# Optimization experiments

Measured on AMD Instinct MI355X. Metric: run time of the kernel, lower is better.

Reference implementation:

```python
import jax, jax.numpy as jnp
import numpy as np

B, S, D, H = 2, 2048, 128, 8  # batch, seq, num_hidden(=head dim), num_heads
EPS = 1e-5


def setup_inputs() -> dict:
    key = jax.random.key(0)
    ks = jax.random.split(key, 12)
    sc = 0.02
    return {
        "query": jax.random.normal(ks[0], (B, S, D), dtype=jnp.float32),
        "Wq": jax.random.normal(ks[1], (2 * H * D, D), dtype=jnp.float32) * sc,
        "bq": jnp.zeros((2 * H * D,), dtype=jnp.float32),
        "Wk": jax.random.normal(ks[2], (2 * H * D, D), dtype=jnp.float32) * sc,
        "bk": jnp.zeros((2 * H * D,), dtype=jnp.float32),
        "Wv": jax.random.normal(ks[3], (H * D, D), dtype=jnp.float32) * sc,
        "bv": jnp.zeros((H * D,), dtype=jnp.float32),
        "Wo": jax.random.normal(ks[4], (D, H * D), dtype=jnp.float32) * sc,
        "bo": jnp.zeros((D,), dtype=jnp.float32),
        "gn_w": jnp.ones((H,), dtype=jnp.float32),
        "gn_b": jnp.zeros((H,), dtype=jnp.float32),
        "lam": jax.random.uniform(ks[5], (), dtype=jnp.float32),
    }


def reference(query, Wq, bq, Wk, bk, Wv, bv, Wo, bo, gn_w, gn_b, lam):
    # Faithful to the torch module: the .view calls are raw reshapes (no
    # transpose), d_k=1 so scale is 1, mask=None path (no causal mask),
    # dropout in eval mode, _lambda == _lambda_init == lam.
    q = (query @ Wq.T + bq).reshape(B, H, S, 2 * D)
    k = (query @ Wk.T + bk).reshape(B, H, S, 2 * D)
    v = (query @ Wv.T + bv).reshape(B, H, S, D)
    q1, q2 = q[..., :D], q[..., D:]
    k1, k2 = k[..., :D], k[..., D:]
    s1 = jnp.einsum("bhqd,bhkd->bhqk", q1, k1)  # / sqrt(d_k=1)
    s2 = jnp.einsum("bhqd,bhkd->bhqk", q2, k2)
    attn = jax.nn.softmax(s1, axis=-1) - lam * jax.nn.softmax(s2, axis=-1)
    out = jnp.einsum("bhqk,bhkd->bhqd", attn, v)          # (B,H,S,D)
    out = out.transpose(0, 2, 1, 3).reshape(B, H, S, D)   # faithful raw reshape
    # GroupNorm(num_groups=H, num_channels=H): normalize per (b, h) over (S, D)
    mean = out.mean(axis=(2, 3), keepdims=True)
    var = out.var(axis=(2, 3), keepdims=True)
    out = (out - mean) * jax.lax.rsqrt(var + EPS)
    out = out * gn_w[None, :, None, None] + gn_b[None, :, None, None]
    out = out * (1.0 - lam)
    # torch.cat([out[:, i] for i in range(H)], dim=-1) -> (B, S, H*D)
    out = out.transpose(0, 2, 1, 3).reshape(B, S, H * D)
    return out @ Wo.T + bo
```

## Files before the change

### kernel.cpp

```cpp
#include <hip/hip_runtime.h>

typedef __bf16 bf16x8 __attribute__((ext_vector_type(8)));
typedef __bf16 bf16x4 __attribute__((ext_vector_type(4)));
typedef float  f32x4  __attribute__((ext_vector_type(4)));

#define MFMA16(a,b,c) __builtin_amdgcn_mfma_f32_16x16x32_bf16((a),(b),(c),0,0,0)

__device__ __forceinline__ bf16x8 cvt8(float4 a, float4 b) {
  bf16x8 v;
  v[0]=(__bf16)a.x; v[1]=(__bf16)a.y; v[2]=(__bf16)a.z; v[3]=(__bf16)a.w;
  v[4]=(__bf16)b.x; v[5]=(__bf16)b.y; v[6]=(__bf16)b.z; v[7]=(__bf16)b.w;
  return v;
}
__device__ __forceinline__ bf16x4 cvt4(float4 a) {
  bf16x4 v;
  v[0]=(__bf16)a.x; v[1]=(__bf16)a.y; v[2]=(__bf16)a.z; v[3]=(__bf16)a.w;
  return v;
}


__global__ void to_bf16(const float* __restrict__ q,  const float* __restrict__ wq,
                        const float* __restrict__ wk, const float* __restrict__ wv,
                        __bf16* __restrict__ qb,  __bf16* __restrict__ wqb,
                        __bf16* __restrict__ wkb, __bf16* __restrict__ wvb)
{
  const long e = (long)(blockIdx.x * 256 + threadIdx.x) * 8;
  const float* src; __bf16* dst; long off;
  if (e < 524288)       { src = q;  dst = qb;  off = e; }
  else if (e < 786432)  { src = wq; dst = wqb; off = e - 524288; }
  else if (e < 1048576) { src = wk; dst = wkb; off = e - 786432; }
  else                  { src = wv; dst = wvb; off = e - 1048576; }
  *(bf16x8*)(dst + off) = cvt8(*(const float4*)(src + off), *(const float4*)(src + off + 4));
}

#define LDA 136
__global__ __launch_bounds__(256, 2) void qkv_gemm(
    const __bf16* __restrict__ queryb,
    const __bf16* __restrict__ Wqb, const float* __restrict__ bq,
    const __bf16* __restrict__ Wkb, const float* __restrict__ bk,
    const __bf16* __restrict__ Wvb, const float* __restrict__ bv,
    __bf16* __restrict__ Qbf, __bf16* __restrict__ Kbf, __bf16* __restrict__ Vbf)
{
  __shared__ __bf16 As[128 * LDA];
  __shared__ __bf16 Bs[128 * LDA];
  const int t = threadIdx.x;
  const int tile = blockIdx.x;
  const int tm = tile / 40, tn = tile % 40;
  const int m0 = tm * 128, n0 = tn * 128;

  const __bf16* wbase; const float* bias;
  __bf16* obase; int ocol0; int ostride; float oscale;
  if (n0 < 2048)      { wbase = Wqb + n0*128;        bias = bq + n0;        obase = Qbf; ocol0 = n0;      ostride = 2048; oscale = 1.4426950408889634f; }
  else if (n0 < 4096) { wbase = Wkb + (n0-2048)*128; bias = bk + (n0-2048); obase = Kbf; ocol0 = n0-2048; ostride = 2048; oscale = 1.0f; }
  else                { wbase = Wvb + (n0-4096)*128; bias = bv + (n0-4096); obase = Vbf; ocol0 = n0-4096; ostride = 1024; oscale = 1.0f; }

  const __bf16* abase = queryb + (long)m0 * 128;
  for (int r = 0; r < 2; ++r) {
    int e = (r*256 + t) * 32;
    int row = e >> 7, col = e & 127;
    #pragma unroll
    for (int c = 0; c < 4; ++c) {
      *(bf16x8*)&As[row*LDA + col + c*8] = *(const bf16x8*)(abase + (long)row*128 + col + c*8);
      *(bf16x8*)&Bs[row*LDA + col + c*8] = *(const bf16x8*)(wbase + (long)row*128 + col + c*8);
    }
  }
  __syncthreads();

  const int w = t >> 6, lane = t & 63;
  const int lo = lane & 15, quad = lane >> 4;
  const int wm = w >> 1, wn = w & 1;

  f32x4 acc[4][4];
  #pragma unroll
  for (int i = 0; i < 4; ++i)
    #pragma unroll
    for (int j = 0; j < 4; ++j) acc[i][j] = (f32x4){0.f,0.f,0.f,0.f};

  #pragma unroll
  for (int ks = 0; ks < 4; ++ks) {
    bf16x8 af[4], bfr[4];
    #pragma unroll
    for (int i = 0; i < 4; ++i)
      af[i] = *(const bf16x8*)&As[(wm*64 + i*16 + lo)*LDA + ks*32 + quad*8];
    #pragma unroll
    for (int j = 0; j < 4; ++j)
      bfr[j] = *(const bf16x8*)&Bs[(wn*64 + j*16 + lo)*LDA + ks*32 + quad*8];
    #pragma unroll
    for (int i = 0; i < 4; ++i)
      #pragma unroll
      for (int j = 0; j < 4; ++j)
        acc[i][j] = MFMA16(bfr[j], af[i], acc[i][j]);
  }
  #pragma unroll
  for (int j = 0; j < 4; ++j) {
    const int colb = ocol0 + wn*64 + j*16 + quad*4;
    const f32x4 b4 = *(const f32x4*)(bias + wn*64 + j*16 + quad*4);
    #pragma unroll
    for (int i = 0; i < 4; ++i) {
      const int row = m0 + wm*64 + i*16 + lo;
      bf16x4 v;
      #pragma unroll
      for (int r = 0; r < 4; ++r) v[r] = (__bf16)((acc[i][j][r] + b4[r]) * oscale);
      *(bf16x4*)&obase[(long)row*ostride + colb] = v;
    }
  }
}

__global__ void v_transpose(const __bf16* __restrict__ Vbf, __bf16* __restrict__ Vt)
{
  __shared__ __bf16 tile[128 * 136];
  const int t = threadIdx.x;
  const int bh = blockIdx.x >> 4, st = blockIdx.x & 15;
  const __bf16* src = Vbf + (long)bh*262144 + st*16384;
  for (int r = 0; r < 8; ++r) {
    int e = (r*256 + t) * 8;
    int row = e >> 7, col = e & 127;
    *(bf16x8*)&tile[row*136 + col] = *(const bf16x8*)(src + row*128 + col);
  }
  __syncthreads();
  __bf16* dst = Vt + (long)bh*262144 + st*128;
  for (int r = 0; r < 8; ++r) {
    int e = (r*256 + t) * 8;
    int d = e >> 7, s2c = e & 127;
    bf16x8 v;
    #pragma unroll
    for (int i = 0; i < 8; ++i) v[i] = tile[(s2c + i)*136 + d];
    *(bf16x8*)(dst + d*2048 + s2c) = v;
  }
}

__global__ __launch_bounds__(256, 2) void attn(
    const __bf16* __restrict__ Qbf, const __bf16* __restrict__ Kbf,
    const __bf16* __restrict__ Vt, float* __restrict__ O,
    const float* __restrict__ lam_p, float* __restrict__ stats)
{
  __shared__ __align__(16) char pool[57344];
  __bf16* Ks  = (__bf16*)pool;
  __bf16* Vs  = (__bf16*)(pool + 32768);
  float*  red = (float*)(pool + 49152);

  const int t = threadIdx.x;
  const int w = t >> 6, lane = t & 63;
  const int lo = lane & 15, quad = lane >> 4;
  const int s = w & 1, qg = w >> 1;
  const int bh = blockIdx.x & 15, qb = blockIdx.x >> 4;
  const float lam = *lam_p;

  const __bf16* Qh = Qbf + (long)bh*524288;
  const __bf16* Kh = Kbf + (long)bh*524288;
  const __bf16* Vh = Vt  + (long)bh*262144;
  const int qrow0 = qb*64 + qg*32;

  bf16x8 qf[2][4];
  #pragma unroll
  for (int qt = 0; qt < 2; ++qt)
    #pragma unroll
    for (int ks = 0; ks < 4; ++ks)
      qf[qt][ks] = *(const bf16x8*)(Qh + (long)(qrow0 + qt*16 + lo)*256 + s*128 + ks*32 + quad*8);

  const int xk = lo & 7;
  int kcolr[4];
  #pragma unroll
  for (int ks = 0; ks < 4; ++ks) kcolr[ks] = ((s*16 + ks*4 + quad) ^ xk) << 3;

  const int vlb = (lo >> 2) * 128;
  const int vc0 = ((4*(lo & 3) + quad) ^ (lo >> 2)) << 3;
  const int vc1 = ((4*(lo & 3) + quad) ^ (lo >> 2) ^ 4) << 3;

  int ke[2], kpos0[2], kpos1[2], vdd[2], vch[2], vpos[2];
  #pragma unroll
  for (int r = 0; r < 2; ++r) {
    ke[r] = (r*256 + t) * 16;
    const int row = ke[r] >> 8;
    const int kcol = ke[r] & 255;
    const int ksrow = (row & 3) + ((row >> 2) & 1)*16 + ((row >> 3) & 3)*4;
    const int sl = kcol >> 3;
    kpos0[r] = ksrow*256 + ((sl       ^ (ksrow & 7)) << 3);
    kpos1[r] = ksrow*256 + (((sl + 1) ^ (ksrow & 7)) << 3);
    const int c = r*256 + t;
    vdd[r] = c >> 2; vch[r] = c & 3;
    const int vrow = vdd[r] >> 2;
    vpos[r] = vrow*128 + ((((vdd[r] & 3) << 2) + vch[r]) ^ (vrow & 7))*8;
  }

  bf16x8 kra[2][2], vra[2];
  #pragma unroll
  for (int r = 0; r < 2; ++r) {
    kra[r][0] = *(const bf16x8*)(Kh + ke[r]);
    kra[r][1] = *(const bf16x8*)(Kh + ke[r] + 8);
    vra[r]    = *(const bf16x8*)(Vh + (long)vdd[r]*2048 + vch[r]*8);
  }
  #pragma unroll
  for (int r = 0; r < 2; ++r) {
    *(bf16x8*)&Ks[kpos0[r]] = kra[r][0];
    *(bf16x8*)&Ks[kpos1[r]] = kra[r][1];
    *(bf16x8*)&Vs[vpos[r]]  = vra[r];
  }

  f32x4 acc[2][8];
  #pragma unroll
  for (int qt = 0; qt < 2; ++qt)
    #pragma unroll
    for (int mt = 0; mt < 8; ++mt) acc[qt][mt] = (f32x4){0.f,0.f,0.f,0.f};
  float lsum[2] = {0.f, 0.f};

  for (int kt = 0; kt < 64; ++kt) {
    __syncthreads();
    if (kt + 1 < 64) {
      #pragma unroll
      for (int r = 0; r < 2; ++r) {
        kra[r][0] = *(const bf16x8*)(Kh + (long)(kt+1)*8192 + ke[r]);
        kra[r][1] = *(const bf16x8*)(Kh + (long)(kt+1)*8192 + ke[r] + 8);
        vra[r]    = *(const bf16x8*)(Vh + (long)vdd[r]*2048 + (kt+1)*32 + vch[r]*8);
      }
    }
    const __bf16* kb = &Ks[(kt & 1) * 8192];
    const __bf16* vb = &Vs[(kt & 1) * 4096];

    f32x4 sf[2][2];
    #pragma unroll
    for (int qt = 0; qt < 2; ++qt)
      #pragma unroll
      for (int nt = 0; nt < 2; ++nt) sf[qt][nt] = (f32x4){0.f,0.f,0.f,0.f};
    #pragma unroll
    for (int nt = 0; nt < 2; ++nt) {
      const int krb = (lo + nt*16) * 256;
      #pragma unroll
      for (int ks = 0; ks < 4; ++ks) {
        bf16x8 kf = *(const bf16x8*)&kb[krb + kcolr[ks]];
        sf[0][nt] = MFMA16(kf, qf[0][ks], sf[0][nt]);
        sf[1][nt] = MFMA16(kf, qf[1][ks], sf[1][nt]);
      }
    }

    bf16x8 pf[2];
    #pragma unroll
    for (int qt = 0; qt < 2; ++qt) {
      #pragma unroll
      for (int nt = 0; nt < 2; ++nt) {
        #pragma unroll
        for (int r = 0; r < 4; ++r) {
          float p = __builtin_exp2f(sf[qt][nt][r]);
          lsum[qt] += p;
          pf[qt][nt*4+r] = (__bf16)p;
        }
      }
    }

    #pragma unroll
    for (int mt = 0; mt < 8; ++mt) {
      bf16x8 vf = *(const bf16x8*)&vb[mt*512 + vlb + ((mt & 1) ? vc1 : vc0)];
      acc[0][mt] = MFMA16(vf, pf[0], acc[0][mt]);
      acc[1][mt] = MFMA16(vf, pf[1], acc[1][mt]);
    }

    if (kt + 1 < 64) {
      __bf16* kn = &Ks[((kt+1) & 1) * 8192];
      __bf16* vn = &Vs[((kt+1) & 1) * 4096];
      #pragma unroll
      for (int r = 0; r < 2; ++r) {
        *(bf16x8*)&kn[kpos0[r]] = kra[r][0];
        *(bf16x8*)&kn[kpos1[r]] = kra[r][1];
        *(bf16x8*)&vn[vpos[r]]  = vra[r];
      }
    }
  }

  #pragma unroll
  for (int qt = 0; qt < 2; ++qt) {
    lsum[qt] += __shfl_xor(lsum[qt], 16);
    lsum[qt] += __shfl_xor(lsum[qt], 32);
  }
  float inv[2];
  const float nume = (s == 0) ? 1.f : lam;
  inv[0] = nume / lsum[0];
  inv[1] = nume / lsum[1];

  float* fs = (float*)pool;
  __syncthreads();
  if (s == 1) {
    #pragma unroll
    for (int qt = 0; qt < 2; ++qt)
      #pragma unroll
      for (int mt = 0; mt < 8; ++mt) {
        f32x4 o;
        #pragma unroll
        for (int r = 0; r < 4; ++r) o[r] = acc[qt][mt][r] * inv[qt];
        *(f32x4*)&fs[(qg*32 + qt*16 + lo)*132 + mt*16 + quad*4] = o;
      }
  }
  __syncthreads();

  float ssum = 0.f, ssq = 0.f;
  if (s == 0) {
    float* Oh = O + (long)bh*262144;
    #pragma unroll
    for (int qt = 0; qt < 2; ++qt)
      #pragma unroll
      for (int mt = 0; mt < 8; ++mt) {
        f32x4 o2 = *(const f32x4*)&fs[(qg*32 + qt*16 + lo)*132 + mt*16 + quad*4];
        f32x4 o;
        #pragma unroll
        for (int r = 0; r < 4; ++r) {
          o[r] = acc[qt][mt][r]*inv[qt] - o2[r];
          ssum += o[r]; ssq += o[r]*o[r];
        }
        *(f32x4*)(Oh + (long)(qrow0 + qt*16 + lo)*128 + mt*16 + quad*4) = o;
      }
  }
  #pragma unroll
  for (int msk = 1; msk < 64; msk <<= 1) { ssum += __shfl_xor(ssum, msk); ssq += __shfl_xor(ssq, msk); }
  if (lane == 0) { red[w] = ssum; red[4 + w] = ssq; }
  __syncthreads();
  if (t == 0) {
    const int g = (bh >> 3)*8 + (qb >> 2);
    atomicAdd(&stats[g*2],   red[0] + red[1] + red[2] + red[3]);
    atomicAdd(&stats[g*2+1], red[4] + red[5] + red[6] + red[7]);
  }
}

#define LDC 72
__global__ __launch_bounds__(256, 2) void out_gemm(
    const float* __restrict__ O, const float* __restrict__ stats,
    const float* __restrict__ gn_w, const float* __restrict__ gn_b,
    const float* __restrict__ lam_p,
    const float* __restrict__ Wo, const float* __restrict__ bo,
    float* __restrict__ out)
{
  __shared__ __bf16 As[64 * LDC];
  __shared__ __bf16 Bs[128 * LDC];
  const int t = threadIdx.x;
  const int w = t >> 6, lane = t & 63;
  const int lo = lane & 15, quad = lane >> 4;
  const int m0 = (blockIdx.x & 63) * 64;
  const int kq = blockIdx.x >> 6;
  const int b = m0 >> 11;
  const float lam1 = 1.f - *lam_p;

  const int hp = kq;
  const float sN   = stats[(b*8 + hp)*2];
  const float ssN  = stats[(b*8 + hp)*2 + 1];
  const float mean = sN * (1.f/262144.f);
  const float rstd = rsqrtf(ssN * (1.f/262144.f) - mean*mean + 1e-5f);
  const float gwv  = gn_w[hp] * rstd * lam1;
  const float shv  = (gn_b[hp] - mean * rstd * gn_w[hp]) * lam1;

  f32x4 acc[8];
  #pragma unroll
  for (int j = 0; j < 8; ++j) acc[j] = (f32x4){0.f,0.f,0.f,0.f};

  for (int kc = 0; kc < 2; ++kc) {
    const int k0 = kq*128 + kc*64;
    const int d0 = kc*64;
    __syncthreads();
    for (int r = 0; r < 4; ++r) {
      int e = r*1024 + t*4;
      int row_l = e >> 6, col_l = e & 63;
      const int spp = (m0 + row_l) & 2047;
      const int h = spp & 7, srow = hp*256 + (spp >> 3);
      float4 v = *(const float4*)(O + ((long)(b*8 + h)*2048 + srow)*128 + d0 + col_l);
      float4 o;
      o.x = v.x*gwv + shv; o.y = v.y*gwv + shv; o.z = v.z*gwv + shv; o.w = v.w*gwv + shv;
      *(bf16x4*)&As[row_l*LDC + col_l] = cvt4(o);
    }
    for (int r = 0; r < 8; ++r) {
      int e = (r*256 + t) * 4;
      int row = e >> 6, col = e & 63;
      *(bf16x4*)&Bs[row*LDC + col] = cvt4(*(const float4*)(Wo + (long)row*1024 + k0 + col));
    }
    __syncthreads();
    #pragma unroll
    for (int ks = 0; ks < 2; ++ks) {
      bf16x8 af = *(const bf16x8*)&As[(w*16 + lo)*LDC + ks*32 + quad*8];
      #pragma unroll
      for (int j = 0; j < 8; ++j) {
        bf16x8 bfr = *(const bf16x8*)&Bs[(j*16 + lo)*LDC + ks*32 + quad*8];
        acc[j] = MFMA16(af, bfr, acc[j]);
      }
    }
  }
  #pragma unroll
  for (int j = 0; j < 8; ++j) {
    const int col = j*16 + lo;
    const float bb = bo[col] * 0.125f;
    #pragma unroll
    for (int r = 0; r < 4; ++r)
      atomicAdd(&out[(long)(m0 + w*16 + quad*4 + r)*128 + col], acc[j][r] + bb);
  }
}

extern "C" void kernel_launch(void* const* d_in, const int* in_sizes, int n_in,
                              void* d_out, int out_size, void* d_ws, size_t ws_size,
                              hipStream_t stream) {
  const float* query = (const float*)d_in[0];
  const float* Wq = (const float*)d_in[1];
  const float* bq = (const float*)d_in[2];
  const float* Wk = (const float*)d_in[3];
  const float* bk = (const float*)d_in[4];
  const float* Wv = (const float*)d_in[5];
  const float* bv = (const float*)d_in[6];
  const float* Wo = (const float*)d_in[7];
  const float* bo = (const float*)d_in[8];
  const float* gn_w = (const float*)d_in[9];
  const float* gn_b = (const float*)d_in[10];
  const float* lam = (const float*)d_in[11];

  char* ws = (char*)d_ws;
  __bf16* Qbf   = (__bf16*)(ws);
  __bf16* Kbf   = (__bf16*)(ws + (16l<<20));
  __bf16* Vbf   = (__bf16*)(ws + (32l<<20));
  __bf16* Vt    = (__bf16*)(ws + (40l<<20));
  float*  O     = (float* )(ws + (48l<<20));
  __bf16* queryb= (__bf16*)(ws + (64l<<20));
  __bf16* Wqb   = (__bf16*)(ws + (65l<<20));
  __bf16* Wkb   = (__bf16*)(ws + (65l<<20) + (512l<<10));
  __bf16* Wvb   = (__bf16*)(ws + (66l<<20));
  float*  stats = (float* )(ws + (66l<<20) + (256l<<10));
  float* out = (float*)d_out;

  to_bf16    <<<dim3(576),  dim3(256), 0, stream>>>(query, Wq, Wk, Wv, queryb, Wqb, Wkb, Wvb);
  qkv_gemm   <<<dim3(1280), dim3(256), 0, stream>>>(queryb, Wqb, bq, Wkb, bk, Wvb, bv, Qbf, Kbf, Vbf);
  v_transpose<<<dim3(256),  dim3(256), 0, stream>>>(Vbf, Vt);
  attn       <<<dim3(512),  dim3(256), 0, stream>>>(Qbf, Kbf, Vt, O, lam, stats);
  out_gemm   <<<dim3(512),  dim3(256), 0, stream>>>(O, stats, gn_w, gn_b, lam, Wo, bo, out);
}
```

Baseline: 207.0 us.

## Software-pipeline attention loop: defer PV MFMA by one tile behind next QK

```diff
diff --git a/kernel.cpp b/kernel.cpp
--- a/kernel.cpp
+++ b/kernel.cpp
@@ -204,67 +204,89 @@
     for (int mt = 0; mt < 8; ++mt) acc[qt][mt] = (f32x4){0.f,0.f,0.f,0.f};
   float lsum[2] = {0.f, 0.f};
 
-  for (int kt = 0; kt < 64; ++kt) {
-    __syncthreads();
-    if (kt + 1 < 64) {
-      #pragma unroll
-      for (int r = 0; r < 2; ++r) {
-        kra[r][0] = *(const bf16x8*)(Kh + (long)(kt+1)*8192 + ke[r]);
-        kra[r][1] = *(const bf16x8*)(Kh + (long)(kt+1)*8192 + ke[r] + 8);
-        vra[r]    = *(const bf16x8*)(Vh + (long)vdd[r]*2048 + (kt+1)*32 + vch[r]*8);
-      }
-    }
-    const __bf16* kb = &Ks[(kt & 1) * 8192];
-    const __bf16* vb = &Vs[(kt & 1) * 4096];
-
-    f32x4 sf[2][2];
-    #pragma unroll
-    for (int qt = 0; qt < 2; ++qt)
-      #pragma unroll
-      for (int nt = 0; nt < 2; ++nt) sf[qt][nt] = (f32x4){0.f,0.f,0.f,0.f};
-    #pragma unroll
-    for (int nt = 0; nt < 2; ++nt) {
-      const int krb = (lo + nt*16) * 256;
-      #pragma unroll
-      for (int ks = 0; ks < 4; ++ks) {
-        bf16x8 kf = *(const bf16x8*)&kb[krb + kcolr[ks]];
-        sf[0][nt] = MFMA16(kf, qf[0][ks], sf[0][nt]);
-        sf[1][nt] = MFMA16(kf, qf[1][ks], sf[1][nt]);
-      }
-    }
-
-    bf16x8 pf[2];
-    #pragma unroll
-    for (int qt = 0; qt < 2; ++qt) {
-      #pragma unroll
-      for (int nt = 0; nt < 2; ++nt) {
-        #pragma unroll
-        for (int r = 0; r < 4; ++r) {
-          float p = __builtin_exp2f(sf[qt][nt][r]);
-          lsum[qt] += p;
-          pf[qt][nt*4+r] = (__bf16)p;
-        }
-      }
-    }
-
-    #pragma unroll
-    for (int mt = 0; mt < 8; ++mt) {
-      bf16x8 vf = *(const bf16x8*)&vb[mt*512 + vlb + ((mt & 1) ? vc1 : vc0)];
-      acc[0][mt] = MFMA16(vf, pf[0], acc[0][mt]);
-      acc[1][mt] = MFMA16(vf, pf[1], acc[1][mt]);
-    }
-
-    if (kt + 1 < 64) {
-      __bf16* kn = &Ks[((kt+1) & 1) * 8192];
-      __bf16* vn = &Vs[((kt+1) & 1) * 4096];
-      #pragma unroll
-      for (int r = 0; r < 2; ++r) {
-        *(bf16x8*)&kn[kpos0[r]] = kra[r][0];
-        *(bf16x8*)&kn[kpos1[r]] = kra[r][1];
-        *(bf16x8*)&vn[vpos[r]]  = vra[r];
-      }
-    }
-  }
+  bf16x8 vfA[8], vfB[8], pfA[2], pfB[2];
+
+#define BODY(KT, VFC, PFC, VFP, PFP, DOPV)                                   \
+  {                                                                          \
+    __syncthreads();                                                         \
+    const int ktn = (KT) + 1;                                                \
+    if (ktn < 64) {                                                          \
+      _Pragma("unroll")                                                      \
+      for (int r = 0; r < 2; ++r) {                                          \
+        kra[r][0] = *(const bf16x8*)(Kh + (long)ktn*8192 + ke[r]);           \
+        kra[r][1] = *(const bf16x8*)(Kh + (long)ktn*8192 + ke[r] + 8);       \
+        vra[r]    = *(const bf16x8*)(Vh + (long)vdd[r]*2048 + ktn*32 + vch[r]*8); \
+      }                                                                      \
+    }                                                                        \
+    const __bf16* kb = &Ks[((KT) & 1) * 8192];                               \
+    const __bf16* vb = &Vs[((KT) & 1) * 4096];                               \
+    _Pragma("unroll")                                                        \
+    for (int mt = 0; mt < 8; ++mt)                                           \
+      VFC[mt] = *(const bf16x8*)&vb[mt*512 + vlb + ((mt & 1) ? vc1 : vc0)];  \
+    bf16x8 kf[2][4];                                                         \
+    _Pragma("unroll")                                                        \
+    for (int nt = 0; nt < 2; ++nt) {                                         \
+      const int krb = (lo + nt*16) * 256;                                    \
+      _Pragma("unroll")                                                      \
+      for (int ks = 0; ks < 4; ++ks)                                         \
+        kf[nt][ks] = *(const bf16x8*)&kb[krb + kcolr[ks]];                   \
+    }                                                                        \
+    if (DOPV) {                                                              \
+      _Pragma("unroll")                                                      \
+      for (int mt = 0; mt < 8; ++mt) {                                       \
+        acc[0][mt] = MFMA16(VFP[mt], PFP[0], acc[0][mt]);                    \
+        acc[1][mt] = MFMA16(VFP[mt], PFP[1], acc[1][mt]);                    \
+      }                                                                      \
+    }                                                                        \
+    f32x4 sf[2][2];                                                          \
+    _Pragma("unroll")                                                        \
+    for (int qt = 0; qt < 2; ++qt)                                           \
+      _Pragma("unroll")                                                      \
+      for (int nt = 0; nt < 2; ++nt) sf[qt][nt] = (f32x4){0.f,0.f,0.f,0.f};  \
+    _Pragma("unroll")                                                        \
+    for (int nt = 0; nt < 2; ++nt) {                                         \
+      _Pragma("unroll")                                                      \
+      for (int ks = 0; ks < 4; ++ks) {                                       \
+        sf[0][nt] = MFMA16(kf[nt][ks], qf[0][ks], sf[0][nt]);                \
+        sf[1][nt] = MFMA16(kf[nt][ks], qf[1][ks], sf[1][nt]);                \
+      }                                                                      \
+    }                                                                        \
+    _Pragma("unroll")                                                        \
+    for (int qt = 0; qt < 2; ++qt) {                                         \
+      _Pragma("unroll")                                                      \
+      for (int nt = 0; nt < 2; ++nt) {                                       \
+        _Pragma("unroll")                                                    \
+        for (int r = 0; r < 4; ++r) {                                        \
+          float p = __builtin_exp2f(sf[qt][nt][r]);                          \
+          lsum[qt] += p;                                                     \
+          PFC[qt][nt*4+r] = (__bf16)p;                                       \
+        }                                                                    \
+      }                                                                      \
+    }                                                                        \
+    if (ktn < 64) {                                                          \
+      __bf16* kn = &Ks[(ktn & 1) * 8192];                                    \
+      __bf16* vn = &Vs[(ktn & 1) * 4096];                                    \
+      _Pragma("unroll")                                                      \
+      for (int r = 0; r < 2; ++r) {                                          \
+        *(bf16x8*)&kn[kpos0[r]] = kra[r][0];                                 \
+        *(bf16x8*)&kn[kpos1[r]] = kra[r][1];                                 \
+        *(bf16x8*)&vn[vpos[r]]  = vra[r];                                    \
+      }                                                                      \
+    }                                                                        \
+  }
+
+  BODY(0, vfA, pfA, vfB, pfB, 0);
+  for (int kt = 1; kt < 63; kt += 2) {
+    BODY(kt,     vfB, pfB, vfA, pfA, 1);
+    BODY(kt + 1, vfA, pfA, vfB, pfB, 1);
+  }
+  BODY(63, vfB, pfB, vfA, pfA, 1);
+  #pragma unroll
+  for (int mt = 0; mt < 8; ++mt) {
+    acc[0][mt] = MFMA16(vfB[mt], pfB[0], acc[0][mt]);
+    acc[1][mt] = MFMA16(vfB[mt], pfB[1], acc[1][mt]);
+  }
+#undef BODY
 
   #pragma unroll
   for (int qt = 0; qt < 2; ++qt) {
```

After: 205.6 us. No clear change (-0.7%).
